# Performance work log

Hardware: AMD Instinct MI355X
Metric: run time of the kernel (lower is better)

## Reference

```python
import jax, jax.numpy as jnp
import numpy as np

STATE_DIM = 256
ACT_LEN = 16
LATENT = 256
ENC = 512
SLOPE = 0.01  # torch.nn.LeakyReLU() default


def _leaky(x):
    return jnp.where(x >= 0, x, SLOPE * x)


def setup_inputs() -> dict:
    key = jax.random.key(0)
    ks = jax.random.split(key, 16)
    B, T = 64, 1024
    D = STATE_DIM + 2 * ACT_LEN
    s = lambda k, shp, fan_in: jax.random.normal(k, shp, dtype=jnp.float32) * (1.0 / np.sqrt(fan_in))
    return {
        "padded_input": jax.random.normal(ks[0], (B, T, D), dtype=jnp.float32),
        # encoder: Linear(state,enc)+leaky, Linear(enc,enc)+leaky, Linear(enc,latent)+leaky
        "enc_w1": s(ks[1], (STATE_DIM, ENC), STATE_DIM), "enc_b1": jnp.zeros((ENC,), jnp.float32),
        "enc_w2": s(ks[2], (ENC, ENC), ENC),             "enc_b2": jnp.zeros((ENC,), jnp.float32),
        "enc_w3": s(ks[3], (ENC, LATENT), ENC),          "enc_b3": jnp.zeros((LATENT,), jnp.float32),
        # latent dynamics (bias-free)
        "A_w": s(ks[4], (LATENT, LATENT), LATENT),
        "B_w": s(ks[5], (ACT_LEN, LATENT), ACT_LEN),
        # decoder: Linear(latent,enc)+leaky, Linear(enc,enc)+leaky, Linear(enc,state)
        "dec_w1": s(ks[6], (LATENT, ENC), LATENT),       "dec_b1": jnp.zeros((ENC,), jnp.float32),
        "dec_w2": s(ks[7], (ENC, ENC), ENC),             "dec_b2": jnp.zeros((ENC,), jnp.float32),
        "dec_w3": s(ks[8], (ENC, STATE_DIM), ENC),       "dec_b3": jnp.zeros((STATE_DIM,), jnp.float32),
    }


def reference(padded_input, enc_w1, enc_b1, enc_w2, enc_b2, enc_w3, enc_b3,
              A_w, B_w, dec_w1, dec_b1, dec_w2, dec_b2, dec_w3, dec_b3):
    # slice features: [state | u_t | u_t1]
    x_t = padded_input[:, :, :STATE_DIM]                       # [B,T,S]
    u_t1 = padded_input[:, :, STATE_DIM + ACT_LEN:]            # [B,T,A]

    # encoder MLP
    h = _leaky(x_t @ enc_w1 + enc_b1)
    h = _leaky(h @ enc_w2 + enc_b2)
    z_t = _leaky(h @ enc_w3 + enc_b3)                          # [B,T,L]

    # reset_probability=0, nwarmup=0: t=0 uses z_t[:,0], then pure recurrence
    # z1[t] = A z1[t-1] + B u_t1[t]
    Bu = u_t1 @ B_w                                            # [B,T,L]

    def step(prev, bu_t):
        new = prev @ A_w + bu_t                                # [B,L]
        return new, new

    _, z1 = jax.lax.scan(step, z_t[:, 0, :], jnp.swapaxes(Bu, 0, 1))
    z_t1 = jnp.swapaxes(z1, 0, 1)                              # [B,T,L]

    # decoder MLP (last layer linear)
    h = _leaky(z_t1 @ dec_w1 + dec_b1)
    h = _leaky(h @ dec_w2 + dec_b2)
    x_t1 = h @ dec_w3 + dec_b3                                 # [B,T,S]
    return x_t1
```

## Files before the change

kernel.cpp:

```cpp
#include <hip/hip_runtime.h>

constexpr int Bb  = 64;
constexpr int Tt  = 1024;
constexpr int Dd  = 288;
constexpr int Ss  = 256;
constexpr int ALa = 16;
constexpr int Ll  = 256;
constexpr int Ee  = 512;
constexpr int CC  = 8;
constexpr int NCh = 128;
constexpr int NSC = 16;
constexpr int SC  = 8;
constexpr int DEC_CHUNKS = 8;
constexpr int DEC_ROWS = (Bb*Tt)/DEC_CHUNKS;

#define LKY(v) ((v) >= 0.f ? (v) : 0.01f*(v))

using f32x4  = __attribute__((ext_vector_type(4))) float;
using short8 = __attribute__((ext_vector_type(8))) short;
typedef unsigned short ushort_t;

__device__ __forceinline__ unsigned short f2bf(float f){
  unsigned int u = __float_as_uint(f);
  u = (u + 0x7fffu + ((u >> 16) & 1u)) >> 16;
  return (unsigned short)u;
}
__device__ __forceinline__ float bf2f(unsigned short h){
  return __uint_as_float(((unsigned int)h) << 16);
}

__global__ __launch_bounds__(256) void enc_dense(
    const float* __restrict__ xin, int xstride,
    const float* __restrict__ W, const float* __restrict__ bias,
    float* __restrict__ out, int K, int N, int act)
{
  int b = blockIdx.x, col0 = blockIdx.y * 32;
  int tid = threadIdx.x;
  int tx = tid & 31, tk = tid >> 5;
  __shared__ float x[512];
  __shared__ float part[8][33];
  for (int k = tid; k < K; k += 256) x[k] = xin[(long)b*xstride + k];
  __syncthreads();
  int j = col0 + tx;
  float p0=0.f,p1=0.f,p2=0.f,p3=0.f;
  int iters = K >> 3;
  #pragma unroll 2
  for (int i = 0; i < iters; i += 4){
    int k0 = tk + 8*i;
    p0 = fmaf(x[k0     ], W[(long)(k0     )*N + j], p0);
    p1 = fmaf(x[k0 +  8], W[(long)(k0 +  8)*N + j], p1);
    p2 = fmaf(x[k0 + 16], W[(long)(k0 + 16)*N + j], p2);
    p3 = fmaf(x[k0 + 24], W[(long)(k0 + 24)*N + j], p3);
  }
  part[tk][tx] = (p0+p1)+(p2+p3);
  __syncthreads();
  if (tid < 32){
    float s = part[0][tid];
    #pragma unroll
    for (int q = 1; q < 8; ++q) s += part[q][tid];
    s += bias[col0 + tid];
    out[b*N + col0 + tid] = act ? LKY(s) : s;
  }
}

__global__ __launch_bounds__(256) void matmul_g(
    const float* __restrict__ X, const float* __restrict__ Y,
    float* __restrict__ Cf, ushort_t* __restrict__ Ch, ushort_t* __restrict__ Cl)
{
  int i = blockIdx.x;
  int tid = threadIdx.x;
  int jg = tid & 63, tk = tid >> 6;
  __shared__ float row[256];
  __shared__ float4 part[4][64];
  if (tid < 256) row[tid] = X[i*256 + tid];
  __syncthreads();
  int j4 = jg*4;
  float4 p0 = make_float4(0,0,0,0), p1 = make_float4(0,0,0,0);
  int kb = tk*64;
  #pragma unroll 4
  for (int k = kb; k < kb+64; k += 2){
    float x0 = row[k], x1 = row[k+1];
    float4 y0 = *(const float4*)&Y[(k  )*256 + j4];
    float4 y1 = *(const float4*)&Y[(k+1)*256 + j4];
    p0.x = fmaf(x0,y0.x,p0.x); p0.y = fmaf(x0,y0.y,p0.y);
    p0.z = fmaf(x0,y0.z,p0.z); p0.w = fmaf(x0,y0.w,p0.w);
    p1.x = fmaf(x1,y1.x,p1.x); p1.y = fmaf(x1,y1.y,p1.y);
    p1.z = fmaf(x1,y1.z,p1.z); p1.w = fmaf(x1,y1.w,p1.w);
  }
  p0.x+=p1.x; p0.y+=p1.y; p0.z+=p1.z; p0.w+=p1.w;
  part[tk][jg] = p0;
  __syncthreads();
  if (tid < 64){
    float4 s = part[0][tid];
    #pragma unroll
    for (int q = 1; q < 4; ++q){
      float4 v = part[q][tid];
      s.x+=v.x; s.y+=v.y; s.z+=v.z; s.w+=v.w;
    }
    int j = tid*4;
    if (Cf) *(float4*)&Cf[i*256 + j] = s;
    if (Ch){
      float vv[4] = {s.x,s.y,s.z,s.w};
      #pragma unroll
      for (int e = 0; e < 4; ++e){
        ushort_t h = f2bf(vv[e]);
        int o = ((i>>3)*256 + j + e)*8 + (i&7);
        Ch[o] = h; Cl[o] = f2bf(vv[e] - bf2f(h));
      }
    }
  }
}

__global__ __launch_bounds__(256) void prep_w(
    const float* __restrict__ W, ushort_t* __restrict__ Wh,
    ushort_t* __restrict__ Wl, int N)
{
  int o = blockIdx.x*256 + threadIdx.x;
  int j = o & 7;
  int rest = o >> 3;
  int n = rest % N;
  int t8 = rest / N;
  int k = t8*8 + j;
  float v = W[k*N + n];
  ushort_t h = f2bf(v);
  Wh[o] = h;
  Wl[o] = f2bf(v - bf2f(h));
}

__global__ __launch_bounds__(256) void prep_bw(
    const float* __restrict__ B, ushort_t* __restrict__ Bh, ushort_t* __restrict__ Bl)
{
  int o = blockIdx.x*256 + threadIdx.x;
  int j = o & 7, rest = o >> 3;
  int n = rest & 255, kq = rest >> 8;
  int k = kq*8 + j;
  float v = (k < ALa) ? B[k*256 + n] : 0.f;
  ushort_t h = f2bf(v);
  Bh[o] = h; Bl[o] = f2bf(v - bf2f(h));
}

__device__ __forceinline__ void load_afrag(
    const ushort_t* __restrict__ P, int kq, int m0, short8* dst)
{
  #pragma unroll
  for (int mt = 0; mt < 4; ++mt)
    dst[mt] = *(const short8*)&P[((long)kq*256 + m0 + mt*16)*8];
}

__global__ __launch_bounds__(256) void scan_mfma(
    const float* __restrict__ in0,
    const ushort_t* __restrict__ AtH, const ushort_t* __restrict__ AtL,
    const ushort_t* __restrict__ BtH, const ushort_t* __restrict__ BtL,
    float* __restrict__ wend, float* __restrict__ zout)
{
  int chunk = blockIdx.x;
  int tid = threadIdx.x;
  int wave = tid >> 6, lane = tid & 63;
  int quad = lane >> 4, l16 = lane & 15;
  int mwave = wave * 64;
  int m0 = mwave + l16;

  __shared__ ushort_t StH[16384];
  __shared__ ushort_t StL[16384];

  short8 Bfh[4], Bfl[4];
  #pragma unroll
  for (int mt = 0; mt < 4; ++mt){
    int off = ((quad)*256 + m0 + mt*16)*8;
    Bfh[mt] = *(const short8*)&BtH[off];
    Bfl[mt] = *(const short8*)&BtL[off];
  }

  f32x4 acc[4][4];
  #pragma unroll
  for (int mt = 0; mt < 4; ++mt)
    #pragma unroll
    for (int nt = 0; nt < 4; ++nt) acc[mt][nt] = (f32x4){0.f,0.f,0.f,0.f};

  const float* ubase[4];
  #pragma unroll
  for (int nt = 0; nt < 4; ++nt)
    ubase[nt] = in0 + (long)(nt*16 + l16)*(Tt*Dd) + (Ss + ALa) + quad*8;

  short8 Ahb[2][4], Alb[2][4];

  for (int tt = 0; tt < CC; ++tt){
    int t = chunk*CC + tt;
    float4 uq[4][2];
    #pragma unroll
    for (int nt = 0; nt < 4; ++nt){
      if (quad < 2){
        const float* up = ubase[nt] + (long)t*Dd;
        uq[nt][0] = *(const float4*)up;
        uq[nt][1] = *(const float4*)(up + 4);
      } else {
        uq[nt][0] = make_float4(0,0,0,0); uq[nt][1] = make_float4(0,0,0,0);
      }
    }

    if (tt > 0){
      load_afrag(AtH, 0*4 + quad, m0, Ahb[0]);
      load_afrag(AtL, 0*4 + quad, m0, Alb[0]);
      #pragma unroll
      for (int kt = 0; kt < 8; ++kt){
        int cur = kt & 1;
        if (kt < 7){
          load_afrag(AtH, (kt+1)*4 + quad, m0, Ahb[cur^1]);
          load_afrag(AtL, (kt+1)*4 + quad, m0, Alb[cur^1]);
        }
        short8 Sbh[4], Sbl[4];
        #pragma unroll
        for (int nt = 0; nt < 4; ++nt){
          int off = ((kt*4 + quad)*64 + nt*16 + l16)*8;
          Sbh[nt] = *(const short8*)&StH[off];
          Sbl[nt] = *(const short8*)&StL[off];
        }
        #pragma unroll
        for (int mt = 0; mt < 4; ++mt)
          #pragma unroll
          for (int nt = 0; nt < 4; ++nt){
            acc[mt][nt] = __builtin_amdgcn_mfma_f32_16x16x32_bf16(Ahb[cur][mt], Sbh[nt], acc[mt][nt], 0,0,0);
            acc[mt][nt] = __builtin_amdgcn_mfma_f32_16x16x32_bf16(Ahb[cur][mt], Sbl[nt], acc[mt][nt], 0,0,0);
            acc[mt][nt] = __builtin_amdgcn_mfma_f32_16x16x32_bf16(Alb[cur][mt], Sbh[nt], acc[mt][nt], 0,0,0);
          }
      }
    }

    short8 uh[4], ul[4];
    #pragma unroll
    for (int nt = 0; nt < 4; ++nt){
      float v[8] = {uq[nt][0].x,uq[nt][0].y,uq[nt][0].z,uq[nt][0].w,
                    uq[nt][1].x,uq[nt][1].y,uq[nt][1].z,uq[nt][1].w};
      ushort_t hs[8], ls[8];
      #pragma unroll
      for (int j = 0; j < 8; ++j){
        hs[j] = f2bf(v[j]);
        ls[j] = f2bf(v[j] - bf2f(hs[j]));
      }
      uh[nt] = *(const short8*)hs; ul[nt] = *(const short8*)ls;
    }
    #pragma unroll
    for (int mt = 0; mt < 4; ++mt)
      #pragma unroll
      for (int nt = 0; nt < 4; ++nt){
        acc[mt][nt] = __builtin_amdgcn_mfma_f32_16x16x32_bf16(Bfh[mt], uh[nt], acc[mt][nt], 0,0,0);
        acc[mt][nt] = __builtin_amdgcn_mfma_f32_16x16x32_bf16(Bfh[mt], ul[nt], acc[mt][nt], 0,0,0);
        acc[mt][nt] = __builtin_amdgcn_mfma_f32_16x16x32_bf16(Bfl[mt], uh[nt], acc[mt][nt], 0,0,0);
      }

    __syncthreads();

    #pragma unroll
    for (int mt = 0; mt < 4; ++mt){
      int mb = mwave + mt*16 + quad*4;
      #pragma unroll
      for (int nt = 0; nt < 4; ++nt){
        int n = nt*16 + l16;
        f32x4 v = acc[mt][nt];
        *(float4*)&zout[((long)n*Tt + t)*Ll + mb] = make_float4(v[0],v[1],v[2],v[3]);
        if (tt == CC-1)
          *(float4*)&wend[((long)chunk*Bb + n)*Ll + mb] = make_float4(v[0],v[1],v[2],v[3]);
        #pragma unroll
        for (int reg = 0; reg < 4; ++reg){
          int m = mb + reg;
          ushort_t h = f2bf(v[reg]);
          ushort_t l = f2bf(v[reg] - bf2f(h));
          int so = ((m>>3)*64 + n)*8 + (m&7);
          StH[so] = h; StL[so] = l;
        }
        acc[mt][nt] = (f32x4){0.f,0.f,0.f,0.f};
      }
    }
    __syncthreads();
  }
}

__global__ __launch_bounds__(256) void pass2_local(
    const float* __restrict__ A8, const float* __restrict__ wend,
    float* __restrict__ lend)
{
  int s = blockIdx.x, rg = blockIdx.y;
  int r = threadIdx.x >> 6, cg = threadIdx.x & 63;
  int b = rg*4 + r;
  __shared__ float cur[4][260];
  float4 l = *(const float4*)&wend[(((SC*s)*Bb) + b)*256 + cg*4];
  *(float4*)&cur[r][cg*4] = l;
  __syncthreads();
  for (int i = 1; i < SC; ++i){
    float4 acc = *(const float4*)&wend[(((SC*s+i)*Bb) + b)*256 + cg*4];
    #pragma unroll 4
    for (int k = 0; k < 256; ++k){
      float lv = cur[r][k];
      float4 a = *(const float4*)&A8[k*256 + cg*4];
      acc.x = fmaf(lv, a.x, acc.x); acc.y = fmaf(lv, a.y, acc.y);
      acc.z = fmaf(lv, a.z, acc.z); acc.w = fmaf(lv, a.w, acc.w);
    }
    __syncthreads();
    *(float4*)&cur[r][cg*4] = acc;
    l = acc;
    __syncthreads();
  }
  *(float4*)&lend[((s*Bb) + b)*256 + cg*4] = l;
}

__global__ __launch_bounds__(256) void pass2_global(
    const float* __restrict__ A64, const float* __restrict__ lend,
    float* __restrict__ inits)
{
  int b = blockIdx.x, tid = threadIdx.x;
  __shared__ float cur[256];
  cur[tid] = inits[b*256 + tid];
  __syncthreads();
  for (int s = 0; s < NSC-1; ++s){
    float p[8] = {0,0,0,0,0,0,0,0};
    #pragma unroll 4
    for (int k = 0; k < 256; k += 8){
      #pragma unroll
      for (int q = 0; q < 8; ++q)
        p[q] = fmaf(cur[k+q], A64[(k+q)*256 + tid], p[q]);
    }
    float acc = lend[((s*Bb) + b)*256 + tid]
              + (((p[0]+p[1])+(p[2]+p[3])) + ((p[4]+p[5])+(p[6]+p[7])));
    __syncthreads();
    cur[tid] = acc;
    inits[((long)((s+1)*SC)*Bb + b)*256 + tid] = acc;
    __syncthreads();
  }
}

__global__ __launch_bounds__(256) void pass2_replay(
    const float* __restrict__ A8, const float* __restrict__ wend,
    float* __restrict__ inits)
{
  int s = blockIdx.x, rg = blockIdx.y;
  int r = threadIdx.x >> 6, cg = threadIdx.x & 63;
  int b = rg*4 + r;
  __shared__ float cur[4][260];
  float4 g = *(const float4*)&inits[(((SC*s)*Bb) + b)*256 + cg*4];
  *(float4*)&cur[r][cg*4] = g;
  __syncthreads();
  for (int i = 0; i < SC-1; ++i){
    float4 acc = *(const float4*)&wend[(((SC*s+i)*Bb) + b)*256 + cg*4];
    #pragma unroll 4
    for (int k = 0; k < 256; ++k){
      float lv = cur[r][k];
      float4 a = *(const float4*)&A8[k*256 + cg*4];
      acc.x = fmaf(lv, a.x, acc.x); acc.y = fmaf(lv, a.y, acc.y);
      acc.z = fmaf(lv, a.z, acc.z); acc.w = fmaf(lv, a.w, acc.w);
    }
    __syncthreads();
    *(float4*)&cur[r][cg*4] = acc;
    *(float4*)&inits[(((SC*s+i+1)*Bb) + b)*256 + cg*4] = acc;
    __syncthreads();
  }
}

__global__ __launch_bounds__(256) void gemm_corr(
    const float* __restrict__ inits, const ushort_t* __restrict__ AjH,
    const ushort_t* __restrict__ AjL, float* __restrict__ out)
{
  int jz = blockIdx.z;
  const ushort_t* Whp = AjH + (long)jz*65536;
  const ushort_t* Wlp = AjL + (long)jz*65536;
  __shared__ __align__(16) ushort_t Xh[4*128*8], Xl[4*128*8];
  __shared__ __align__(16) ushort_t Wh[4*128*8], Wl[4*128*8];

  int tid  = threadIdx.x;
  int wave = tid >> 6, lane = tid & 63;
  int wm = wave & 1, wn = wave >> 1;
  int quad = lane >> 4, l16 = lane & 15;
  int row0 = blockIdx.y * 128;
  int col0 = blockIdx.x * 128;

  f32x4 acc[4][4];
  #pragma unroll
  for (int mt = 0; mt < 4; ++mt)
    #pragma unroll
    for (int nt = 0; nt < 4; ++nt) acc[mt][nt] = (f32x4){0.f,0.f,0.f,0.f};

  for (int kt = 0; kt < 8; ++kt){
    #pragma unroll
    for (int it = 0; it < 2; ++it){
      int idx = tid + it*256;
      int q = idx >> 7, m = idx & 127;
      const float* xp = &inits[(long)(row0 + m)*256 + kt*32 + q*8];
      float4 v0 = *(const float4*)xp;
      float4 v1 = *(const float4*)(xp + 4);
      float vv[8] = {v0.x,v0.y,v0.z,v0.w,v1.x,v1.y,v1.z,v1.w};
      ushort_t hs[8], ls[8];
      #pragma unroll
      for (int j = 0; j < 8; ++j){
        hs[j] = f2bf(vv[j]);
        ls[j] = f2bf(vv[j] - bf2f(hs[j]));
      }
      *(uint4*)&Xh[(q*128 + m)*8] = *(const uint4*)hs;
      *(uint4*)&Xl[(q*128 + m)*8] = *(const uint4*)ls;
      int n = idx & 127;
      long src = (long)(kt*4 + q)*256 + col0 + n;
      ((uint4*)Wh)[q*128 + n] = ((const uint4*)Whp)[src];
      ((uint4*)Wl)[q*128 + n] = ((const uint4*)Wlp)[src];
    }
    __syncthreads();
    short8 ah[4], al[4], bh[4], bl[4];
    #pragma unroll
    for (int mt = 0; mt < 4; ++mt){
      int off = (quad*128 + wm*64 + mt*16 + l16)*8;
      ah[mt] = *(const short8*)&Xh[off];
      al[mt] = *(const short8*)&Xl[off];
    }
    #pragma unroll
    for (int nt = 0; nt < 4; ++nt){
      int off = (quad*128 + wn*64 + nt*16 + l16)*8;
      bh[nt] = *(const short8*)&Wh[off];
      bl[nt] = *(const short8*)&Wl[off];
    }
    #pragma unroll
    for (int mt = 0; mt < 4; ++mt)
      #pragma unroll
      for (int nt = 0; nt < 4; ++nt){
        acc[mt][nt] = __builtin_amdgcn_mfma_f32_16x16x32_bf16(ah[mt], bh[nt], acc[mt][nt], 0,0,0);
        acc[mt][nt] = __builtin_amdgcn_mfma_f32_16x16x32_bf16(ah[mt], bl[nt], acc[mt][nt], 0,0,0);
        acc[mt][nt] = __builtin_amdgcn_mfma_f32_16x16x32_bf16(al[mt], bh[nt], acc[mt][nt], 0,0,0);
      }
    __syncthreads();
  }

  #pragma unroll
  for (int mt = 0; mt < 4; ++mt){
    #pragma unroll
    for (int nt = 0; nt < 4; ++nt){
      int col = col0 + wn*64 + nt*16 + l16;
      #pragma unroll
      for (int reg = 0; reg < 4; ++reg){
        int row = row0 + wm*64 + mt*16 + quad*4 + reg;
        int b = row & 63, c = row >> 6;
        int t = c*CC + jz;
        long addr = ((long)b*Tt + t)*Ll + col;
        out[addr] += acc[mt][nt][reg];
      }
    }
  }
}

template<int BM, int BN, bool INS, bool OUTS>
__global__ __launch_bounds__(256) void gemm_mfma(
    const float* __restrict__ X,
    const ushort_t* __restrict__ Xhp, const ushort_t* __restrict__ Xlp,
    const ushort_t* __restrict__ Whp, const ushort_t* __restrict__ Wlp,
    const float* __restrict__ bias, float* __restrict__ Y,
    ushort_t* __restrict__ Yh, ushort_t* __restrict__ Yl,
    int Mrows, int K, int N, int act)
{
  constexpr int BMh = BM/2, BNh = BN/2;
  constexpr int MT = BM/32, NT = BN/32;
  __shared__ __align__(16) ushort_t Xh[4*BM*8], Xl[4*BM*8];
  __shared__ __align__(16) ushort_t Wh[4*BN*8], Wl[4*BN*8];

  int tid  = threadIdx.x;
  int wave = tid >> 6, lane = tid & 63;
  int wm = wave & 1, wn = wave >> 1;
  int quad = lane >> 4, l16 = lane & 15;
  long row0 = (long)blockIdx.y * BM;
  int col0 = blockIdx.x * BN;

  f32x4 acc[MT][NT];
  #pragma unroll
  for (int mt = 0; mt < MT; ++mt)
    #pragma unroll
    for (int nt = 0; nt < NT; ++nt) acc[mt][nt] = (f32x4){0.f,0.f,0.f,0.f};

  for (int kt = 0; kt < K; kt += 32){
    int ktile = kt >> 5;
    if constexpr (INS){
      #pragma unroll
      for (int it = 0; it < (BM*4)/256; ++it){
        int idx = tid + it*256;
        int q = idx / BM, m = idx % BM;
        long src = (long)(ktile*4 + q)*Mrows + row0 + m;
        ((uint4*)Xh)[q*BM + m] = ((const uint4*)Xhp)[src];
        ((uint4*)Xl)[q*BM + m] = ((const uint4*)Xlp)[src];
      }
    } else {
      #pragma unroll
      for (int it = 0; it < (BM*4)/256; ++it){
        int idx = tid + it*256;
        int q = idx / BM, m = idx % BM;
        const float* xp = &X[(row0 + m)*(long)K + kt + q*8];
        float4 v0 = *(const float4*)xp;
        float4 v1 = *(const float4*)(xp + 4);
        float vv[8] = {v0.x,v0.y,v0.z,v0.w,v1.x,v1.y,v1.z,v1.w};
        ushort_t hs[8], ls[8];
        #pragma unroll
        for (int j = 0; j < 8; ++j){
          hs[j] = f2bf(vv[j]);
          ls[j] = f2bf(vv[j] - bf2f(hs[j]));
        }
        *(uint4*)&Xh[(q*BM + m)*8] = *(const uint4*)hs;
        *(uint4*)&Xl[(q*BM + m)*8] = *(const uint4*)ls;
      }
    }
    #pragma unroll
    for (int it = 0; it < (BN*4)/256; ++it){
      int idx = tid + it*256;
      int q = idx / BN, n = idx % BN;
      long src = (long)(ktile*4 + q)*N + col0 + n;
      ((uint4*)Wh)[q*BN + n] = ((const uint4*)Whp)[src];
      ((uint4*)Wl)[q*BN + n] = ((const uint4*)Wlp)[src];
    }
    __syncthreads();

    short8 ah[MT], al[MT], bh[NT], bl[NT];
    #pragma unroll
    for (int mt = 0; mt < MT; ++mt){
      int off = (quad*BM + wm*BMh + mt*16 + l16)*8;
      ah[mt] = *(const short8*)&Xh[off];
      al[mt] = *(const short8*)&Xl[off];
    }
    #pragma unroll
    for (int nt = 0; nt < NT; ++nt){
      int off = (quad*BN + wn*BNh + nt*16 + l16)*8;
      bh[nt] = *(const short8*)&Wh[off];
      bl[nt] = *(const short8*)&Wl[off];
    }
    #pragma unroll
    for (int mt = 0; mt < MT; ++mt)
      #pragma unroll
      for (int nt = 0; nt < NT; ++nt){
        acc[mt][nt] = __builtin_amdgcn_mfma_f32_16x16x32_bf16(ah[mt], bh[nt], acc[mt][nt], 0, 0, 0);
        acc[mt][nt] = __builtin_amdgcn_mfma_f32_16x16x32_bf16(ah[mt], bl[nt], acc[mt][nt], 0, 0, 0);
        acc[mt][nt] = __builtin_amdgcn_mfma_f32_16x16x32_bf16(al[mt], bh[nt], acc[mt][nt], 0, 0, 0);
      }
    __syncthreads();
  }

  #pragma unroll
  for (int mt = 0; mt < MT; ++mt){
    long rowb = row0 + wm*BMh + mt*16 + quad*4;
    #pragma unroll
    for (int nt = 0; nt < NT; ++nt){
      int col = col0 + wn*BNh + nt*16 + l16;
      float bs = bias[col];
      #pragma unroll
      for (int reg = 0; reg < 4; ++reg){
        float y = acc[mt][nt][reg] + bs;
        if (act) y = LKY(y);
        long row = rowb + reg;
        if constexpr (OUTS){
          ushort_t h = f2bf(y);
          ushort_t l = f2bf(y - bf2f(h));
          long off = ((long)(col >> 3)*Mrows + row)*8 + (col & 7);
          Yh[off] = h; Yl[off] = l;
        } else {
          Y[row*(long)N + col] = y;
        }
      }
    }
  }
}

extern "C" void kernel_launch(void* const* d_in, const int* in_sizes, int n_in,
                              void* d_out, int out_size, void* d_ws, size_t ws_size,
                              hipStream_t stream) {
  const float* in0    = (const float*)d_in[0];
  const float* enc_w1 = (const float*)d_in[1];
  const float* enc_b1 = (const float*)d_in[2];
  const float* enc_w2 = (const float*)d_in[3];
  const float* enc_b2 = (const float*)d_in[4];
  const float* enc_w3 = (const float*)d_in[5];
  const float* enc_b3 = (const float*)d_in[6];
  const float* A_w    = (const float*)d_in[7];
  const float* B_w    = (const float*)d_in[8];
  const float* dec_w1 = (const float*)d_in[9];
  const float* dec_b1 = (const float*)d_in[10];
  const float* dec_w2 = (const float*)d_in[11];
  const float* dec_b2 = (const float*)d_in[12];
  const float* dec_w3 = (const float*)d_in[13];
  const float* dec_b3 = (const float*)d_in[14];
  float* out = (float*)d_out;

  float* ws    = (float*)d_ws;
  float* h1enc = ws;
  float* h2enc = ws + 32768;
  float* s2    = ws + 65536;
  float* s3    = ws + 131072;
  float* s4    = ws + 196608;
  float* s8    = ws + 262144;
  float* s16   = ws + 327680;
  float* s32   = ws + 393216;
  float* s64   = ws + 458752;
  ushort_t* Whp_d = (ushort_t*)(ws + 524288);
  ushort_t* Wlp_d = (ushort_t*)(ws + 786432);
  float* Rf    = ws + 1048576;
  ushort_t* AjH = (ushort_t*)Rf;
  ushort_t* AjL = (ushort_t*)(Rf + 262144);
  ushort_t* BtH = (ushort_t*)(Rf + 524288);
  ushort_t* BtL = BtH + 8192;
  float* wend  = Rf + 532480;
  float* inits = Rf + 2629632;
  float* lend  = Rf + 4726784;
  ushort_t* h1h = (ushort_t*)Rf;
  ushort_t* h1l = (ushort_t*)(Rf + 2097152);
  ushort_t* h2h = (ushort_t*)(Rf + 4194304);
  ushort_t* h2l = (ushort_t*)(Rf + 6291456);

  enc_dense<<<dim3(64,16), 256, 0, stream>>>(in0, Tt*Dd, enc_w1, enc_b1, h1enc, 256, 512, 1);
  enc_dense<<<dim3(64,16), 256, 0, stream>>>(h1enc, 512, enc_w2, enc_b2, h2enc, 512, 512, 1);
  enc_dense<<<dim3(64, 8), 256, 0, stream>>>(h2enc, 512, enc_w3, enc_b3, inits, 512, 256, 1);

  prep_w<<<256, 256, 0, stream>>>(A_w, AjH, AjL, 256);
  prep_bw<<<32, 256, 0, stream>>>(B_w, BtH, BtL);
  matmul_g<<<256, 256, 0, stream>>>(A_w, A_w, s2, AjH+1*65536, AjL+1*65536);
  matmul_g<<<256, 256, 0, stream>>>(s2, A_w, s3, AjH+2*65536, AjL+2*65536);
  matmul_g<<<256, 256, 0, stream>>>(s2, s2, s4, AjH+3*65536, AjL+3*65536);
  matmul_g<<<256, 256, 0, stream>>>(s4, A_w, nullptr, AjH+4*65536, AjL+4*65536);
  matmul_g<<<256, 256, 0, stream>>>(s4, s2, nullptr, AjH+5*65536, AjL+5*65536);
  matmul_g<<<256, 256, 0, stream>>>(s4, s3, nullptr, AjH+6*65536, AjL+6*65536);
  matmul_g<<<256, 256, 0, stream>>>(s4, s4, s8, AjH+7*65536, AjL+7*65536);
  matmul_g<<<256, 256, 0, stream>>>(s8, s8, s16, nullptr, nullptr);
  matmul_g<<<256, 256, 0, stream>>>(s16, s16, s32, nullptr, nullptr);
  matmul_g<<<256, 256, 0, stream>>>(s32, s32, s64, nullptr, nullptr);

  prep_w<<<512,  256, 0, stream>>>(dec_w1, Whp_d,          Wlp_d,          512);
  prep_w<<<1024, 256, 0, stream>>>(dec_w2, Whp_d + 131072, Wlp_d + 131072, 512);
  prep_w<<<512,  256, 0, stream>>>(dec_w3, Whp_d + 393216, Wlp_d + 393216, 256);

  scan_mfma<<<NCh, 256, 0, stream>>>(in0, AjH, AjL, BtH, BtL, wend, out);
  pass2_local <<<dim3(NSC, 16), 256, 0, stream>>>(s8, wend, lend);
  pass2_global<<<64,            256, 0, stream>>>(s64, lend, inits);
  pass2_replay<<<dim3(NSC, 16), 256, 0, stream>>>(s8, wend, inits);
  gemm_corr<<<dim3(2, 64, 8), 256, 0, stream>>>(inits, AjH, AjL, out);

  for (int rc = 0; rc < DEC_CHUNKS; ++rc){
    const float* zc = out + (long)rc*DEC_ROWS*Ll;
    float* oc       = out + (long)rc*DEC_ROWS*Ll;
    gemm_mfma<64,128,false,true><<<dim3(Ee/128, DEC_ROWS/64), 256, 0, stream>>>(
        zc, nullptr, nullptr, Whp_d, Wlp_d, dec_b1, nullptr, h1h, h1l, DEC_ROWS, Ll, Ee, 1);
    gemm_mfma<64,128,true,true><<<dim3(Ee/128, DEC_ROWS/64), 256, 0, stream>>>(
        nullptr, h1h, h1l, Whp_d + 131072, Wlp_d + 131072, dec_b2, nullptr, h2h, h2l, DEC_ROWS, Ee, Ee, 1);
    gemm_mfma<64,128,true,false><<<dim3(Ss/128, DEC_ROWS/64), 256, 0, stream>>>(
        nullptr, h2h, h2l, Whp_d + 393216, Wlp_d + 393216, dec_b3, oc, nullptr, nullptr, DEC_ROWS, Ee, Ss, 0);
  }
}
```

Before: 1.014 ms.

## Rewrite pass-2 carry propagation kernels as split-bf16 MFMA matmuls

The three pass-2 kernels that propagate chunk-boundary states (local, global, replay) were scalar FP32 FMA loops over one batch row group per block. They are now MFMA-based: the 64-batch state is kept in LDS as hi/lo bf16 fragments and multiplied by precomputed bf16 hi/lo splits of A^8 and A^64 with three MFMAs per tile. This targets the serial latency of the recurrence steps, especially the single-block global pass. In exchange it launches far fewer blocks (16 and 1 instead of 256 and 64), adds conversion overhead, and the split-bf16 arithmetic may shift accuracy slightly.

Result: slower. 1.039 ms (+2.5%).

```diff
diff --git a/kernel.cpp b/kernel.cpp
--- a/kernel.cpp
+++ b/kernel.cpp
@@ -275,84 +275,143 @@
   }
 }
 
-__global__ __launch_bounds__(256) void pass2_local(
-    const float* __restrict__ A8, const float* __restrict__ wend,
-    float* __restrict__ lend)
-{
-  int s = blockIdx.x, rg = blockIdx.y;
-  int r = threadIdx.x >> 6, cg = threadIdx.x & 63;
-  int b = rg*4 + r;
-  __shared__ float cur[4][260];
-  float4 l = *(const float4*)&wend[(((SC*s)*Bb) + b)*256 + cg*4];
-  *(float4*)&cur[r][cg*4] = l;
-  __syncthreads();
-  for (int i = 1; i < SC; ++i){
-    float4 acc = *(const float4*)&wend[(((SC*s+i)*Bb) + b)*256 + cg*4];
-    #pragma unroll 4
-    for (int k = 0; k < 256; ++k){
-      float lv = cur[r][k];
-      float4 a = *(const float4*)&A8[k*256 + cg*4];
-      acc.x = fmaf(lv, a.x, acc.x); acc.y = fmaf(lv, a.y, acc.y);
-      acc.z = fmaf(lv, a.z, acc.z); acc.w = fmaf(lv, a.w, acc.w);
-    }
-    __syncthreads();
-    *(float4*)&cur[r][cg*4] = acc;
-    l = acc;
-    __syncthreads();
-  }
-  *(float4*)&lend[((s*Bb) + b)*256 + cg*4] = l;
-}
-
-__global__ __launch_bounds__(256) void pass2_global(
-    const float* __restrict__ A64, const float* __restrict__ lend,
-    float* __restrict__ inits)
-{
-  int b = blockIdx.x, tid = threadIdx.x;
-  __shared__ float cur[256];
-  cur[tid] = inits[b*256 + tid];
-  __syncthreads();
-  for (int s = 0; s < NSC-1; ++s){
-    float p[8] = {0,0,0,0,0,0,0,0};
-    #pragma unroll 4
-    for (int k = 0; k < 256; k += 8){
-      #pragma unroll
-      for (int q = 0; q < 8; ++q)
-        p[q] = fmaf(cur[k+q], A64[(k+q)*256 + tid], p[q]);
-    }
-    float acc = lend[((s*Bb) + b)*256 + tid]
-              + (((p[0]+p[1])+(p[2]+p[3])) + ((p[4]+p[5])+(p[6]+p[7])));
-    __syncthreads();
-    cur[tid] = acc;
-    inits[((long)((s+1)*SC)*Bb + b)*256 + tid] = acc;
-    __syncthreads();
-  }
-}
-
-__global__ __launch_bounds__(256) void pass2_replay(
-    const float* __restrict__ A8, const float* __restrict__ wend,
-    float* __restrict__ inits)
-{
-  int s = blockIdx.x, rg = blockIdx.y;
-  int r = threadIdx.x >> 6, cg = threadIdx.x & 63;
-  int b = rg*4 + r;
-  __shared__ float cur[4][260];
-  float4 g = *(const float4*)&inits[(((SC*s)*Bb) + b)*256 + cg*4];
-  *(float4*)&cur[r][cg*4] = g;
-  __syncthreads();
-  for (int i = 0; i < SC-1; ++i){
-    float4 acc = *(const float4*)&wend[(((SC*s+i)*Bb) + b)*256 + cg*4];
-    #pragma unroll 4
-    for (int k = 0; k < 256; ++k){
-      float lv = cur[r][k];
-      float4 a = *(const float4*)&A8[k*256 + cg*4];
-      acc.x = fmaf(lv, a.x, acc.x); acc.y = fmaf(lv, a.y, acc.y);
-      acc.z = fmaf(lv, a.z, acc.z); acc.w = fmaf(lv, a.w, acc.w);
-    }
-    __syncthreads();
-    *(float4*)&cur[r][cg*4] = acc;
-    *(float4*)&inits[(((SC*s+i+1)*Bb) + b)*256 + cg*4] = acc;
-    __syncthreads();
-  }
+__device__ __forceinline__ void frag_init_state(
+    const float* __restrict__ src, ushort_t* StH, ushort_t* StL, int tid)
+{
+  #pragma unroll
+  for (int it = 0; it < 8; ++it){
+    int idx = tid + it*256;
+    int m8 = idx >> 6, n = idx & 63;
+    const float* p = src + (long)n*256 + m8*8;
+    float4 v0 = *(const float4*)p;
+    float4 v1 = *(const float4*)(p + 4);
+    float vv[8] = {v0.x,v0.y,v0.z,v0.w,v1.x,v1.y,v1.z,v1.w};
+    ushort_t hs[8], ls[8];
+    #pragma unroll
+    for (int j = 0; j < 8; ++j){
+      hs[j] = f2bf(vv[j]);
+      ls[j] = f2bf(vv[j] - bf2f(hs[j]));
+    }
+    *(uint4*)&StH[(m8*64 + n)*8] = *(const uint4*)hs;
+    *(uint4*)&StL[(m8*64 + n)*8] = *(const uint4*)ls;
+  }
+}
+
+__device__ __forceinline__ void p2_step(
+    const ushort_t* __restrict__ PH, const ushort_t* __restrict__ PL,
+    const float* __restrict__ addin,
+    ushort_t* StH, ushort_t* StL,
+    float* __restrict__ out_f32,
+    int wave, int lane)
+{
+  int quad = lane >> 4, l16 = lane & 15;
+  int mwave = wave*64, m0 = mwave + l16;
+
+  f32x4 acc[4][4];
+  #pragma unroll
+  for (int mt = 0; mt < 4; ++mt){
+    int mb = mwave + mt*16 + quad*4;
+    #pragma unroll
+    for (int nt = 0; nt < 4; ++nt){
+      int n = nt*16 + l16;
+      float4 v = *(const float4*)&addin[(long)n*256 + mb];
+      acc[mt][nt] = (f32x4){v.x, v.y, v.z, v.w};
+    }
+  }
+
+  short8 Ahb[2][4], Alb[2][4];
+  load_afrag(PH, 0*4 + quad, m0, Ahb[0]);
+  load_afrag(PL, 0*4 + quad, m0, Alb[0]);
+  #pragma unroll
+  for (int kt = 0; kt < 8; ++kt){
+    int cur = kt & 1;
+    if (kt < 7){
+      load_afrag(PH, (kt+1)*4 + quad, m0, Ahb[cur^1]);
+      load_afrag(PL, (kt+1)*4 + quad, m0, Alb[cur^1]);
+    }
+    short8 Sbh[4], Sbl[4];
+    #pragma unroll
+    for (int nt = 0; nt < 4; ++nt){
+      int off = ((kt*4 + quad)*64 + nt*16 + l16)*8;
+      Sbh[nt] = *(const short8*)&StH[off];
+      Sbl[nt] = *(const short8*)&StL[off];
+    }
+    #pragma unroll
+    for (int mt = 0; mt < 4; ++mt)
+      #pragma unroll
+      for (int nt = 0; nt < 4; ++nt){
+        acc[mt][nt] = __builtin_amdgcn_mfma_f32_16x16x32_bf16(Ahb[cur][mt], Sbh[nt], acc[mt][nt], 0,0,0);
+        acc[mt][nt] = __builtin_amdgcn_mfma_f32_16x16x32_bf16(Ahb[cur][mt], Sbl[nt], acc[mt][nt], 0,0,0);
+        acc[mt][nt] = __builtin_amdgcn_mfma_f32_16x16x32_bf16(Alb[cur][mt], Sbh[nt], acc[mt][nt], 0,0,0);
+      }
+  }
+
+  __syncthreads();
+
+  #pragma unroll
+  for (int mt = 0; mt < 4; ++mt){
+    int mb = mwave + mt*16 + quad*4;
+    #pragma unroll
+    for (int nt = 0; nt < 4; ++nt){
+      int n = nt*16 + l16;
+      f32x4 v = acc[mt][nt];
+      if (out_f32)
+        *(float4*)&out_f32[(long)n*256 + mb] = make_float4(v[0],v[1],v[2],v[3]);
+      #pragma unroll
+      for (int reg = 0; reg < 4; ++reg){
+        int m = mb + reg;
+        ushort_t h = f2bf(v[reg]);
+        int so = ((m>>3)*64 + n)*8 + (m&7);
+        StH[so] = h;
+        StL[so] = f2bf(v[reg] - bf2f(h));
+      }
+    }
+  }
+  __syncthreads();
+}
+
+__global__ __launch_bounds__(256) void pass2_local_mfma(
+    const ushort_t* __restrict__ A8H, const ushort_t* __restrict__ A8L,
+    const float* __restrict__ wend, float* __restrict__ lend)
+{
+  int s = blockIdx.x;
+  int tid = threadIdx.x;
+  int wave = tid >> 6, lane = tid & 63;
+  __shared__ ushort_t StH[16384], StL[16384];
+  frag_init_state(wend + (long)(s*SC)*Bb*256, StH, StL, tid);
+  __syncthreads();
+  for (int i = 1; i < SC; ++i)
+    p2_step(A8H, A8L, wend + (long)(s*SC + i)*Bb*256, StH, StL,
+            (i == SC-1) ? (lend + (long)s*Bb*256) : nullptr, wave, lane);
+}
+
+__global__ __launch_bounds__(256) void pass2_global_mfma(
+    const ushort_t* __restrict__ A64H, const ushort_t* __restrict__ A64L,
+    const float* __restrict__ lend, float* __restrict__ inits)
+{
+  int tid = threadIdx.x;
+  int wave = tid >> 6, lane = tid & 63;
+  __shared__ ushort_t StH[16384], StL[16384];
+  frag_init_state(inits, StH, StL, tid);
+  __syncthreads();
+  for (int s = 0; s < NSC-1; ++s)
+    p2_step(A64H, A64L, lend + (long)s*Bb*256, StH, StL,
+            inits + (long)((s+1)*SC)*Bb*256, wave, lane);
+}
+
+__global__ __launch_bounds__(256) void pass2_replay_mfma(
+    const ushort_t* __restrict__ A8H, const ushort_t* __restrict__ A8L,
+    const float* __restrict__ wend, float* __restrict__ inits)
+{
+  int s = blockIdx.x;
+  int tid = threadIdx.x;
+  int wave = tid >> 6, lane = tid & 63;
+  __shared__ ushort_t StH[16384], StL[16384];
+  frag_init_state(inits + (long)(s*SC)*Bb*256, StH, StL, tid);
+  __syncthreads();
+  for (int i = 0; i < SC-1; ++i)
+    p2_step(A8H, A8L, wend + (long)(s*SC + i)*Bb*256, StH, StL,
+            inits + (long)(s*SC + i + 1)*Bb*256, wave, lane);
 }
 
 __global__ __launch_bounds__(256) void gemm_corr(
@@ -598,10 +657,14 @@
   float* wend  = Rf + 532480;
   float* inits = Rf + 2629632;
   float* lend  = Rf + 4726784;
+  ushort_t* A64H = (ushort_t*)(Rf + 4988928);
+  ushort_t* A64L = (ushort_t*)(Rf + 5021696);
   ushort_t* h1h = (ushort_t*)Rf;
   ushort_t* h1l = (ushort_t*)(Rf + 2097152);
   ushort_t* h2h = (ushort_t*)(Rf + 4194304);
   ushort_t* h2l = (ushort_t*)(Rf + 6291456);
+  ushort_t* A8H = AjH + 7*65536;
+  ushort_t* A8L = AjL + 7*65536;
 
   enc_dense<<<dim3(64,16), 256, 0, stream>>>(in0, Tt*Dd, enc_w1, enc_b1, h1enc, 256, 512, 1);
   enc_dense<<<dim3(64,16), 256, 0, stream>>>(h1enc, 512, enc_w2, enc_b2, h2enc, 512, 512, 1);
@@ -615,19 +678,19 @@
   matmul_g<<<256, 256, 0, stream>>>(s4, A_w, nullptr, AjH+4*65536, AjL+4*65536);
   matmul_g<<<256, 256, 0, stream>>>(s4, s2, nullptr, AjH+5*65536, AjL+5*65536);
   matmul_g<<<256, 256, 0, stream>>>(s4, s3, nullptr, AjH+6*65536, AjL+6*65536);
-  matmul_g<<<256, 256, 0, stream>>>(s4, s4, s8, AjH+7*65536, AjL+7*65536);
+  matmul_g<<<256, 256, 0, stream>>>(s4, s4, s8, A8H, A8L);
   matmul_g<<<256, 256, 0, stream>>>(s8, s8, s16, nullptr, nullptr);
   matmul_g<<<256, 256, 0, stream>>>(s16, s16, s32, nullptr, nullptr);
-  matmul_g<<<256, 256, 0, stream>>>(s32, s32, s64, nullptr, nullptr);
+  matmul_g<<<256, 256, 0, stream>>>(s32, s32, s64, A64H, A64L);
 
   prep_w<<<512,  256, 0, stream>>>(dec_w1, Whp_d,          Wlp_d,          512);
   prep_w<<<1024, 256, 0, stream>>>(dec_w2, Whp_d + 131072, Wlp_d + 131072, 512);
   prep_w<<<512,  256, 0, stream>>>(dec_w3, Whp_d + 393216, Wlp_d + 393216, 256);
 
   scan_mfma<<<NCh, 256, 0, stream>>>(in0, AjH, AjL, BtH, BtL, wend, out);
-  pass2_local <<<dim3(NSC, 16), 256, 0, stream>>>(s8, wend, lend);
-  pass2_global<<<64,            256, 0, stream>>>(s64, lend, inits);
-  pass2_replay<<<dim3(NSC, 16), 256, 0, stream>>>(s8, wend, inits);
+  pass2_local_mfma <<<NSC, 256, 0, stream>>>(A8H, A8L, wend, lend);
+  pass2_global_mfma<<<1,   256, 0, stream>>>(A64H, A64L, lend, inits);
+  pass2_replay_mfma<<<NSC, 256, 0, stream>>>(A8H, A8L, wend, inits);
   gemm_corr<<<dim3(2, 64, 8), 256, 0, stream>>>(inits, AjH, AjL, out);
 
   for (int rc = 0; rc < DEC_CHUNKS; ++rc){
```
